# Optimization experiments

Hardware: AMD Instinct MI355X
Metric: run time of the kernel (lower is better)

Reference implementation:

```python
import jax, jax.numpy as jnp
import numpy as np

G = 4           # graphs in batch
NV_PER = 3000   # variables per graph
NC_PER = 1000   # constraints per graph
DEG = 8         # constraint neighbors per variable
D_FEAT = 64
D_HID = 128
D_OUT = 64
K_BREAK = 8     # n_breakings
EPS = 1e-5


def setup_inputs() -> dict:
    key = jax.random.key(0)
    ks = jax.random.split(key, 5)
    nv, nc = G * NV_PER, G * NC_PER
    # bipartite edges: each variable connects to DEG random constraints within its graph
    var = np.tile(np.repeat(np.arange(NV_PER), DEG), G) + np.repeat(np.arange(G) * NV_PER, NV_PER * DEG)
    con = np.asarray(jax.random.randint(ks[0], (G, NV_PER * DEG), 0, NC_PER)) + (np.arange(G) * NC_PER)[:, None]
    con = con.reshape(-1)
    edge_indices = jnp.asarray(np.stack([con, var]), dtype=jnp.int32)            # (constraint, variable)
    reversed_edge_indices = jnp.asarray(np.stack([var, con]), dtype=jnp.int32)   # (variable, constraint)
    return {
        'variable_features': jax.random.normal(ks[1], (nv, D_FEAT), jnp.float32),
        'constraint_features': jax.random.normal(ks[2], (nc, D_FEAT), jnp.float32),
        'W1': jax.random.normal(ks[3], (D_FEAT + 1, D_HID), jnp.float32) * (1.0 / np.sqrt(D_FEAT + 1)),
        'b1': jnp.zeros((D_HID,), jnp.float32),
        'W2': jax.random.normal(ks[4], (D_HID, D_OUT), jnp.float32) * (1.0 / np.sqrt(D_HID)),
        'b2': jnp.zeros((D_OUT,), jnp.float32),
        'gamma': jnp.ones((D_OUT,), jnp.float32),
        'beta': jnp.zeros((D_OUT,), jnp.float32),
        'edge_indices': edge_indices,
        'reversed_edge_indices': reversed_edge_indices,
        'n_variables_per_graph': jnp.full((G,), NV_PER, jnp.int32),
        'n_constraints_per_graph': jnp.full((G,), NC_PER, jnp.int32),
    }


def _build_adj(edge_indices, reversed_edge_indices, nv, N):
    # homogeneous symmetric bipartite adjacency + gcn_norm(add_self_loops=True)
    rows = jnp.concatenate([reversed_edge_indices[0], edge_indices[0] + nv])
    cols = jnp.concatenate([reversed_edge_indices[1] + nv, edge_indices[1]])
    deg = jax.ops.segment_sum(jnp.ones_like(rows, jnp.float32), rows, num_segments=N) + 1.0
    dinv = jax.lax.rsqrt(deg)
    edge_vals = dinv[rows] * dinv[cols]     # D^-1/2 A D^-1/2 off-diagonal
    loop_vals = dinv * dinv                  # self-loop diagonal
    return rows, cols, edge_vals, loop_vals


def _spmm(rows, cols, edge_vals, loop_vals, N, X):
    # X: (N, d) -> adj @ X
    return jax.ops.segment_sum(edge_vals[:, None] * X[cols], rows, num_segments=N) + loop_vals[:, None] * X


def _holo_forward(variable_features, constraint_features, W1, b1, W2, b2, gamma, beta,
                  rows, cols, edge_vals, loop_vals, break_idx, break_group, G_):
    nv = variable_features.shape[0]
    N = nv + constraint_features.shape[0]
    nvp = nv // G_
    X = jnp.concatenate([variable_features, constraint_features], axis=0)        # (N, d)
    B = break_idx.shape[0]
    one_hot = jax.nn.one_hot(break_idx, N, dtype=X.dtype)                        # (B, N)
    Xb = jnp.concatenate([jnp.broadcast_to(X, (B,) + X.shape), one_hot[:, :, None]], axis=-1)  # (B, N, d+1)
    spmm = lambda x: _spmm(rows, cols, edge_vals, loop_vals, N, x)
    h = jax.nn.relu(jax.lax.map(spmm, Xb @ W1 + b1))                             # (B, N, D_HID)
    out = jax.lax.map(spmm, h @ W2 + b2)                                         # (B, N, D_OUT)
    mu = out.mean(-1, keepdims=True)
    var = ((out - mu) ** 2).mean(-1, keepdims=True)
    holo = (out - mu) * jax.lax.rsqrt(var + EPS) * gamma + beta                  # LayerNorm
    set_link = holo[:, :nv, :]                                                   # r=1: tuples = variables
    global_mean = set_link.mean(0)                                               # (nv, D_OUT)
    tuple_group = jnp.repeat(jnp.arange(G_), nvp)                                # (nv,)
    group_sum = jax.ops.segment_sum(set_link, break_group, num_segments=G_)      # (G, nv, D_OUT)
    counts = jax.ops.segment_sum(jnp.ones((B,), holo.dtype), break_group, num_segments=G_)
    link = group_sum[tuple_group, jnp.arange(nv)] / jnp.maximum(counts[tuple_group], 1.0)[:, None]
    return jnp.where((counts[tuple_group] > 0)[:, None], link, global_mean)


def reference(variable_features, constraint_features, W1, b1, W2, b2, gamma, beta,
              edge_indices, reversed_edge_indices, n_variables_per_graph, n_constraints_per_graph):
    nv = variable_features.shape[0]
    nc = constraint_features.shape[0]
    N = nv + nc
    G_ = n_variables_per_graph.shape[0]
    nvp, ncp = nv // G_, nc // G_
    rows, cols, edge_vals, loop_vals = _build_adj(edge_indices, reversed_edge_indices, nv, N)
    node_degrees = jax.ops.segment_sum(edge_vals, rows, num_segments=N) + loop_vals  # adj row sums
    # per-graph top-k degree nodes (tie-expansion is measure-zero for float gcn-norm degrees)
    var_ids = jnp.arange(G_)[:, None] * nvp + jnp.arange(nvp)[None, :]
    con_ids = nv + jnp.arange(G_)[:, None] * ncp + jnp.arange(ncp)[None, :]
    sample_nodes = jnp.concatenate([var_ids, con_ids], axis=1)                   # (G, nvp+ncp)
    _, local = jax.lax.top_k(node_degrees[sample_nodes], K_BREAK)
    break_idx = jnp.take_along_axis(sample_nodes, local, axis=1).reshape(-1)     # (G*K,)
    break_group = jnp.repeat(jnp.arange(G_), K_BREAK)
    return _holo_forward(variable_features, constraint_features, W1, b1, W2, b2, gamma, beta,
                         rows, cols, edge_vals, loop_vals, break_idx, break_group, G_)
```

## Files before the change

kernel.cpp:

```cpp
#include <hip/hip_runtime.h>
#include <hip/hip_bf16.h>

#define G_      4
#define NVP     3000
#define NCP     1000
#define DEG     8
#define NV      (G_*NVP)
#define NC      (G_*NCP)
#define NN      (NV+NC)
#define NE      (NV*DEG)
#define EPG     (NVP*DEG)
#define DF      64
#define DH      128
#define DO      64
#define KB      8
#define NB      (G_*KB)
#define MAXR    96
#define MAXJ    640
#define FWD2_GEMM_BLOCKS (NV/32)

__global__ __launch_bounds__(1024) void k_setup(const int* __restrict__ conArr,
    int* __restrict__ csr_off, int* __restrict__ csr_cur,
    float* __restrict__ dinvC_g, float* __restrict__ nodeval, int* __restrict__ breakix)
{
    __shared__ int   cnt[NCP];
    __shared__ float dinvC[NCP];
    __shared__ float nvl[NVP + NCP];
    __shared__ int   wsum[16];
    __shared__ float mv[16]; __shared__ int mp[16];

    int g = blockIdx.x, tid = threadIdx.x, lane = tid & 63, w = tid >> 6;
    int ebase = g * EPG, cb = g * NCP;
    const float dv3 = 1.0f/3.0f;

    if (tid < NCP) cnt[tid] = 0;
    __syncthreads();
    for (int e = tid; e < EPG; e += 1024)
        atomicAdd(&cnt[conArr[ebase + e] - cb], 1);
    __syncthreads();
    int x = (tid < NCP) ? cnt[tid] : 0;
    int orig = x;
    for (int o = 1; o < 64; o <<= 1) { int y = __shfl_up(x, o); if (lane >= o) x += y; }
    if (lane == 63) wsum[w] = x;
    __syncthreads();
    if (tid == 0) { int run = 0; for (int t = 0; t < 16; ++t) { int z = wsum[t]; wsum[t] = run; run += z; } }
    __syncthreads();
    int excl = x - orig + wsum[w];
    if (tid < NCP) {
        csr_off[cb + tid] = ebase + excl;
        csr_cur[cb + tid] = ebase + excl;
        float dc = 1.0f / sqrtf((float)(orig + 1));
        dinvC[tid] = dc;
        dinvC_g[cb + tid] = dc;
        float nvc = (float)orig * (dc * dv3) + dc*dc;
        nvl[NVP + tid] = nvc;
        nodeval[NV + cb + tid] = nvc;
    }
    if (g == 0 && tid == 0) csr_off[NC] = NE;
    __syncthreads();
    for (int v = tid; v < NVP; v += 1024) {
        float s = 0.f;
        int e0 = ebase + v*DEG;
        #pragma unroll
        for (int k = 0; k < DEG; ++k) s += dv3 * dinvC[conArr[e0+k] - cb];
        float val = s + dv3*dv3;
        nvl[v] = val;
        nodeval[g*NVP + v] = val;
    }
    __syncthreads();
    for (int it = 0; it < KB; ++it) {
        float bv = -1e30f; int bp = 1 << 30;
        for (int p = tid; p < NVP+NCP; p += 1024) {
            float vv = nvl[p];
            if (vv > bv || (vv == bv && p < bp)) { bv = vv; bp = p; }
        }
        for (int o = 32; o > 0; o >>= 1) {
            float ov = __shfl_xor(bv, o); int op = __shfl_xor(bp, o);
            if (ov > bv || (ov == bv && op < bp)) { bv = ov; bp = op; }
        }
        if (lane == 0) { mv[w] = bv; mp[w] = bp; }
        __syncthreads();
        if (tid == 0) {
            float fv = mv[0]; int fp = mp[0];
            for (int t = 1; t < 16; ++t)
                if (mv[t] > fv || (mv[t] == fv && mp[t] < fp)) { fv = mv[t]; fp = mp[t]; }
            nvl[fp] = -1e30f;
            breakix[g*KB + it] = (fp < NVP) ? (g*NVP + fp) : (NV + g*NCP + (fp - NVP));
        }
        __syncthreads();
    }
}

__global__ __launch_bounds__(1024) void k_fill(const int* __restrict__ conArr,
                                               int* __restrict__ csr_cur,
                                               int* __restrict__ csr_v) {
    int e = blockIdx.x*1024 + threadIdx.x;
    if (e < NE) { int p = atomicAdd(&csr_cur[conArr[e]], 1); csr_v[p] = e >> 3; }
}

__global__ void k_spmmX(const float* __restrict__ vf, const float* __restrict__ cf,
                        const float* __restrict__ dinvC, const int* __restrict__ conArr,
                        const int* __restrict__ csr_off, const int* __restrict__ csr_v,
                        float* __restrict__ AX)
{
    int i = blockIdx.x*4 + (threadIdx.x >> 6);
    int lane = threadIdx.x & 63;
    const float dv3 = 1.0f/3.0f;
    float acc, di;
    if (i < NV) {
        di = dv3;
        acc = dv3 * vf[(size_t)i*DF + lane];
        int e0 = i*DEG;
        #pragma unroll
        for (int k = 0; k < DEG; ++k) {
            int c = conArr[e0+k];
            acc += dinvC[c] * cf[(size_t)c*DF + lane];
        }
    } else {
        int c = i - NV;
        di = dinvC[c];
        float base = di * cf[(size_t)c*DF + lane];
        int p0 = csr_off[c], p1 = csr_off[c+1];
        int len = p1 - p0;
        int myv = (p0 + lane < p1) ? csr_v[p0 + lane] : 0;
        int lim = len < 64 ? len : 64;
        float a0 = 0.f, a1 = 0.f, a2 = 0.f, a3 = 0.f;
        int m = 0;
        for (; m + 4 <= lim; m += 4) {
            int v0 = __shfl(myv, m+0);
            int v1 = __shfl(myv, m+1);
            int v2 = __shfl(myv, m+2);
            int v3 = __shfl(myv, m+3);
            a0 += vf[(size_t)v0*DF + lane];
            a1 += vf[(size_t)v1*DF + lane];
            a2 += vf[(size_t)v2*DF + lane];
            a3 += vf[(size_t)v3*DF + lane];
        }
        for (; m < lim; ++m) { int v = __shfl(myv, m); a0 += vf[(size_t)v*DF + lane]; }
        for (int p = p0 + 64; p < p1; ++p) a0 += vf[(size_t)csr_v[p]*DF + lane];
        acc = base + dv3 * ((a0 + a1) + (a2 + a3));
    }
    AX[(size_t)i*DF + lane] = di * acc;
}

__global__ __launch_bounds__(256) void k_gemm1(const float* __restrict__ AX, const float* __restrict__ W1,
                        const float* __restrict__ b1, const float* __restrict__ nodeval,
                        float* __restrict__ S1)
{
    __shared__ float W1T[128*68];
    __shared__ float AXs[32*68];
    int tid = threadIdx.x;
    for (int t = tid; t < 64*128; t += 256) {
        int k = t >> 7, c = t & 127;
        W1T[c*68 + k] = W1[t];
    }
    int r0 = blockIdx.x * 32;
    for (int t = tid; t < 32*16; t += 256) {
        int row = t >> 4, q = t & 15;
        *(float4*)&AXs[row*68 + q*4] = *(const float4*)&AX[(size_t)(r0+row)*DF + q*4];
    }
    __syncthreads();
    int tc = tid & 15, tr = tid >> 4;
    float acc[2][8];
    #pragma unroll
    for (int r = 0; r < 2; ++r)
        #pragma unroll
        for (int j = 0; j < 8; ++j) acc[r][j] = 0.f;
    #pragma unroll
    for (int k0 = 0; k0 < 64; k0 += 4) {
        float4 a0 = *(const float4*)&AXs[(tr*2+0)*68 + k0];
        float4 a1 = *(const float4*)&AXs[(tr*2+1)*68 + k0];
        #pragma unroll
        for (int j = 0; j < 8; ++j) {
            float4 wv = *(const float4*)&W1T[(tc + 16*j)*68 + k0];
            acc[0][j] += a0.x*wv.x + a0.y*wv.y + a0.z*wv.z + a0.w*wv.w;
            acc[1][j] += a1.x*wv.x + a1.y*wv.y + a1.z*wv.z + a1.w*wv.w;
        }
    }
    #pragma unroll
    for (int r = 0; r < 2; ++r) {
        int row = r0 + tr*2 + r;
        float nv_ = nodeval[row];
        #pragma unroll
        for (int j = 0; j < 8; ++j) {
            int col = tc + 16*j;
            S1[(size_t)row*DH + col] = acc[r][j] + nv_*b1[col];
        }
    }
}

__global__ void k_spmmH(const float* __restrict__ S1, const float* __restrict__ dinvC,
                        const int* __restrict__ conArr, float* __restrict__ AH)
{
    int v = blockIdx.x*2 + (threadIdx.x >> 7);
    int ch = threadIdx.x & 127;
    const float dv3 = 1.0f/3.0f;
    float acc = dv3 * fmaxf(S1[(size_t)v*DH + ch], 0.f);
    int e0 = v*DEG;
    #pragma unroll
    for (int k = 0; k < DEG; ++k) {
        int c = conArr[e0+k];
        acc += dinvC[c] * fmaxf(S1[(size_t)(NV + c)*DH + ch], 0.f);
    }
    AH[(size_t)v*DH + ch] = dv3 * acc;
}

__global__ __launch_bounds__(256) void k_fwd2(const float* __restrict__ S1,
    const float* __restrict__ AH,
    const float* __restrict__ dinvC, const int* __restrict__ conArr,
    const int* __restrict__ csr_off, const int* __restrict__ csr_v,
    const float* __restrict__ W1, const float* __restrict__ W2,
    const float* __restrict__ b2, const float* __restrict__ nodeval,
    const float* __restrict__ gamma, const float* __restrict__ beta,
    const int* __restrict__ breakidx,
    float* __restrict__ outvar, float* __restrict__ holo, float* __restrict__ out,
    int* __restrict__ RnG, float* __restrict__ RwG, int* __restrict__ nRG,
    float* __restrict__ dz2G)
{
    __shared__ float smem[14848];
    __shared__ int nR_s;
    int tid = threadIdx.x, lane = tid & 63, w = tid >> 6;
    const float dv3 = 1.0f/3.0f;

    if (blockIdx.x < FWD2_GEMM_BLOCKS) {
        float* W2T = smem;
        float* AHs = smem + 8448;
        float* s2  = smem + 12672;
        for (int t = tid; t < 128*64; t += 256) {
            int k = t >> 6, c = t & 63;
            W2T[c*132 + k] = W2[t];
        }
        int r0 = blockIdx.x * 32;
        for (int t = tid; t < 32*32; t += 256) {
            int row = t >> 5, q = t & 31;
            *(float4*)&AHs[row*132 + q*4] = *(const float4*)&AH[(size_t)(r0+row)*DH + q*4];
        }
        __syncthreads();
        int tc = tid & 15, tr = tid >> 4;
        float acc[2][4];
        #pragma unroll
        for (int r = 0; r < 2; ++r)
            #pragma unroll
            for (int j = 0; j < 4; ++j) acc[r][j] = 0.f;
        #pragma unroll
        for (int k0 = 0; k0 < 128; k0 += 4) {
            float4 a0 = *(const float4*)&AHs[(tr*2+0)*132 + k0];
            float4 a1 = *(const float4*)&AHs[(tr*2+1)*132 + k0];
            #pragma unroll
            for (int j = 0; j < 4; ++j) {
                float4 wv = *(const float4*)&W2T[(tc + 16*j)*132 + k0];
                acc[0][j] += a0.x*wv.x + a0.y*wv.y + a0.z*wv.z + a0.w*wv.w;
                acc[1][j] += a1.x*wv.x + a1.y*wv.y + a1.z*wv.z + a1.w*wv.w;
            }
        }
        #pragma unroll
        for (int r = 0; r < 2; ++r) {
            int row = tr*2 + r;
            float nv_ = nodeval[r0 + row];
            #pragma unroll
            for (int j = 0; j < 4; ++j) {
                int col = tc + 16*j;
                s2[row*68 + col] = acc[r][j] + nv_*b2[col];
            }
        }
        __syncthreads();
        float gm = gamma[lane], bt = beta[lane];
        for (int rr = 0; rr < 8; ++rr) {
            int row = w*8 + rr;
            int v = r0 + row;
            float xv = s2[row*68 + lane];
            float s = xv;
            for (int o = 32; o > 0; o >>= 1) s += __shfl_xor(s, o);
            float mu = s * (1.f/64.f);
            float d = xv - mu;
            float vs = d*d;
            for (int o = 32; o > 0; o >>= 1) vs += __shfl_xor(vs, o);
            float rstd = 1.0f / sqrtf(vs*(1.f/64.f) + 1e-5f);
            float h = d*rstd*gm + bt;
            outvar[(size_t)v*DO + lane] = xv;
            holo  [(size_t)v*DO + lane] = h;
            out   [(size_t)v*DO + lane] = h;
        }
    } else {
        float* W2s = smem;
        float* dh  = smem + 8192;
        float* Rw  = smem + 8704;
        int*   Rn  = (int*)(smem + 8800);
        int b = blockIdx.x - FWD2_GEMM_BLOCKS;
        int i = breakidx[b];
        for (int t = tid; t < 128*64; t += 256) W2s[t] = W2[t];
        if (tid < 64) {
            if (i >= NV) {
                int c = i - NV;
                float di = dinvC[c];
                int p0 = csr_off[c], len = csr_off[c+1] - p0;
                if (len <= 64) {
                    int v = (lane < len) ? csr_v[p0 + lane] : 0x7fffffff;
                    int firstLane = 64, mult = 0;
                    for (int m = 0; m < 64; ++m) {
                        int vm = __shfl(v, m);
                        if (vm == v) { mult++; if (m < firstLane) firstLane = m; }
                    }
                    bool head = (lane < len) && (firstLane == lane);
                    unsigned long long hmask = __ballot(head);
                    int hrk = 0;
                    for (int m = 0; m < 64; ++m) {
                        if (!((hmask >> m) & 1)) continue;
                        int vm = __shfl(v, m);
                        if (vm < v) hrk++;
                    }
                    if (head) { Rn[hrk] = v; Rw[hrk] = (float)mult * (dv3 * di); }
                    int nH = __popcll(hmask);
                    if (lane == 0) { Rn[nH] = i; Rw[nH] = di*di; nR_s = nH + 1; }
                } else if (lane == 0) {
                    int n = 0;
                    for (int p = p0; p < p0 + len; ++p) {
                        int v = csr_v[p]; int f = -1;
                        for (int q = 0; q < n; ++q) if (Rn[q] == v) { f = q; break; }
                        if (f >= 0) Rw[f] += dv3 * di;
                        else if (n < MAXR-1) { Rn[n] = v; Rw[n] = dv3 * di; ++n; }
                    }
                    Rn[n] = i; Rw[n] = di*di; nR_s = n + 1;
                }
            } else if (lane == 0) {
                float di = dv3;
                int cn[DEG];
                for (int k = 0; k < DEG; ++k) cn[k] = NV + conArr[i*DEG + k];
                for (int a = 1; a < DEG; ++a) { int key = cn[a]; int bb = a-1;
                    while (bb >= 0 && cn[bb] > key) { cn[bb+1] = cn[bb]; --bb; } cn[bb+1] = key; }
                int n = 0, k = 0;
                while (k < DEG) { int u = cn[k]; int m = 1; ++k;
                    while (k < DEG && cn[k] == u) { ++m; ++k; }
                    Rn[n] = u; Rw[n] = (float)m * dinvC[u - NV] * di; ++n; }
                Rn[n] = i; Rw[n] = di*di; nR_s = n + 1;
            }
        }
        __syncthreads();
        int nR = nR_s;
        for (int t = tid; t < nR; t += 256) { RnG[b*MAXR + t] = Rn[t]; RwG[b*MAXR + t] = Rw[t]; }
        if (tid == 0) nRG[b] = nR;
        for (int r0 = 0; r0 < nR; r0 += 4) {
            __syncthreads();
            for (int t = tid; t < 512; t += 256) {
                int ty = t >> 7, k = t & 127;
                int r = r0 + ty;
                if (r < nR) {
                    float s1 = S1[(size_t)Rn[r]*DH + k];
                    float a = s1 + Rw[r] * W1[64*128 + k];
                    dh[ty*128 + k] = fmaxf(a, 0.f) - fmaxf(s1, 0.f);
                }
            }
            __syncthreads();
            int ty2 = tid >> 6, c2 = tid & 63;
            int r2 = r0 + ty2;
            if (r2 < nR) {
                float accv = 0.f;
                #pragma unroll
                for (int kk = 0; kk < 128; ++kk) accv += dh[ty2*128 + kk] * W2s[kk*64 + c2];
                dz2G[((size_t)b*MAXR + r2)*DO + c2] = accv;
            }
        }
    }
}

__global__ __launch_bounds__(256) void k_corr_b(const int* __restrict__ RnG, const float* __restrict__ RwG,
                         const int* __restrict__ nRG, const float* __restrict__ dz2G,
                         const int* __restrict__ breakidx, const float* __restrict__ dinvC,
                         const int* __restrict__ conArr, const int* __restrict__ csr_off,
                         const int* __restrict__ csr_v,
                         const float* __restrict__ outvar, const float* __restrict__ holo,
                         const float* __restrict__ gamma, const float* __restrict__ beta,
                         float* __restrict__ out) {
    int b = blockIdx.x;
    int lane = threadIdx.x & 63, wv = threadIdx.x >> 6;
    const float dv3 = 1.0f/3.0f;
    __shared__ int Jn[MAXJ];
    __shared__ int nJ_s;
    int i = breakidx[b];
    int nR = nRG[b];
    float gm = gamma[lane], bt = beta[lane];
    if (i >= NV) {
        int nJ = nR - 1;
        const float* dzi = &dz2G[((size_t)b*MAXR + (nR-1))*DO];
        for (int j0 = wv; j0 < nJ; j0 += 4) {
            int j = RnG[b*MAXR + j0];
            float aji = RwG[b*MAXR + j0];
            float x = outvar[(size_t)j*DO + lane]
                    + aji * dzi[lane]
                    + dv3*dv3 * dz2G[((size_t)b*MAXR + j0)*DO + lane];
            float s = x; for (int o = 32; o > 0; o >>= 1) s += __shfl_xor(s, o);
            float mu = s * (1.f/64.f);
            float d = x - mu;
            float vs = d*d; for (int o = 32; o > 0; o >>= 1) vs += __shfl_xor(vs, o);
            float rstd = 1.0f / sqrtf(vs*(1.f/64.f) + 1e-5f);
            float hn = d*rstd*gm + bt;
            atomicAdd(&out[(size_t)j*DO + lane], 0.125f * (hn - holo[(size_t)j*DO + lane]));
        }
    } else {
        if (threadIdx.x == 0) {
            int n = 0; Jn[n++] = i;
            for (int r = 0; r < nR-1; ++r) {
                int c = RnG[b*MAXR + r] - NV;
                for (int p = csr_off[c]; p < csr_off[c+1]; ++p) {
                    int u = csr_v[p];
                    bool found = false;
                    for (int q = 0; q < n; ++q) if (Jn[q] == u) { found = true; break; }
                    if (!found && n < MAXJ) Jn[n++] = u;
                }
            }
            nJ_s = n;
        }
        __syncthreads();
        int nJ = nJ_s;
        for (int j0 = wv; j0 < nJ; j0 += 4) {
            int j = Jn[j0];
            float x = outvar[(size_t)j*DO + lane];
            for (int k = 0; k < DEG; ++k) {
                int cn = NV + conArr[j*DEG + k];
                for (int r = 0; r < nR-1; ++r)
                    if (RnG[b*MAXR + r] == cn) {
                        x += dv3 * dinvC[cn - NV] * dz2G[((size_t)b*MAXR + r)*DO + lane];
                        break;
                    }
            }
            if (j == i) x += dv3*dv3 * dz2G[((size_t)b*MAXR + nR-1)*DO + lane];
            float s = x; for (int o = 32; o > 0; o >>= 1) s += __shfl_xor(s, o);
            float mu = s * (1.f/64.f);
            float d = x - mu;
            float vs = d*d; for (int o = 32; o > 0; o >>= 1) vs += __shfl_xor(vs, o);
            float rstd = 1.0f / sqrtf(vs*(1.f/64.f) + 1e-5f);
            float hn = d*rstd*gm + bt;
            atomicAdd(&out[(size_t)j*DO + lane], 0.125f * (hn - holo[(size_t)j*DO + lane]));
        }
    }
}


extern "C" void kernel_launch(void* const* d_in, const int* in_sizes, int n_in,
                              void* d_out, int out_size, void* d_ws, size_t ws_size,
                              hipStream_t stream) {
    const float* vf    = (const float*)d_in[0];
    const float* cf    = (const float*)d_in[1];
    const float* W1    = (const float*)d_in[2];
    const float* b1    = (const float*)d_in[3];
    const float* W2    = (const float*)d_in[4];
    const float* b2    = (const float*)d_in[5];
    const float* gamma = (const float*)d_in[6];
    const float* beta  = (const float*)d_in[7];
    const int*   ei    = (const int*)d_in[8];
    const int*   conArr = ei;
    float* out = (float*)d_out;

    char* ws = (char*)d_ws;
    size_t off = 0;
    auto alloc = [&](size_t bytes) { char* p = ws + off; off = (off + bytes + 255) & ~(size_t)255; return p; };
    float* dinvC   = (float*)alloc(NC*4);
    int*   csr_off = (int*)  alloc((NC+1)*4);
    int*   csr_cur = (int*)  alloc(NC*4);
    int*   csr_v   = (int*)  alloc(NE*4);
    float* nodeval = (float*)alloc(NN*4);
    int*   breakix = (int*)  alloc(NB*4);
    float* AX      = (float*)alloc((size_t)NN*DF*4);
    float* S1      = (float*)alloc((size_t)NN*DH*4);
    float* AH      = (float*)alloc((size_t)NV*DH*4);
    float* outvar  = (float*)alloc((size_t)NV*DO*4);
    float* holo    = (float*)alloc((size_t)NV*DO*4);
    int*   RnG     = (int*)  alloc(NB*MAXR*4);
    float* RwG     = (float*)alloc(NB*MAXR*4);
    int*   nRG     = (int*)  alloc(NB*4);
    float* dz2G    = (float*)alloc((size_t)NB*MAXR*DO*4);

    k_setup <<<G_, 1024, 0, stream>>>(conArr, csr_off, csr_cur, dinvC, nodeval, breakix);
    k_fill  <<<(NE+1023)/1024, 1024, 0, stream>>>(conArr, csr_cur, csr_v);
    k_spmmX <<<NN/4, 256, 0, stream>>>(vf, cf, dinvC, conArr, csr_off, csr_v, AX);
    k_gemm1 <<<NN/32, 256, 0, stream>>>(AX, W1, b1, nodeval, S1);
    k_spmmH <<<NV/2, 256, 0, stream>>>(S1, dinvC, conArr, AH);
    k_fwd2  <<<FWD2_GEMM_BLOCKS + NB, 256, 0, stream>>>(S1, AH, dinvC, conArr, csr_off, csr_v,
                                       W1, W2, b2, nodeval, gamma, beta, breakix,
                                       outvar, holo, out, RnG, RwG, nRG, dz2G);
    k_corr_b<<<NB, 256, 0, stream>>>(RnG, RwG, nRG, dz2G, breakix, dinvC, conArr,
                                     csr_off, csr_v, outvar, holo, gamma, beta, out);
}
```

Before: 108.2 us.

## Fuse sparse aggregations into GEMM kernels and widen blocks to 1024 threads

Merges the feature aggregation (A·X) into the first GEMM kernel and the hidden aggregation (A·relu(H)) into the second GEMM kernel, so each 32-row tile is built in shared memory instead of going through the global AX and AH buffers. This removes two kernel launches and the global write/read round trips for those intermediates. Blocks grow to 1024 threads, with one output per thread in the GEMM stage and 8 rows per step in the correction stage. The cost is fewer resident blocks per CU, larger register and LDS pressure per block, and a dh buffer region enlarged to hold 8 rows.

After: 95.37 us, median of 2. 1.13x faster.

```diff
diff --git a/kernel.cpp b/kernel.cpp
--- a/kernel.cpp
+++ b/kernel.cpp
@@ -17,7 +17,7 @@
 #define NB      (G_*KB)
 #define MAXR    96
 #define MAXJ    640
-#define FWD2_GEMM_BLOCKS (NV/32)
+#define F2_GEMM_BLOCKS (NV/32)
 
 __global__ __launch_bounds__(1024) void k_setup(const int* __restrict__ conArr,
     int* __restrict__ csr_off, int* __restrict__ csr_cur,
@@ -98,115 +98,81 @@
     if (e < NE) { int p = atomicAdd(&csr_cur[conArr[e]], 1); csr_v[p] = e >> 3; }
 }
 
-__global__ void k_spmmX(const float* __restrict__ vf, const float* __restrict__ cf,
-                        const float* __restrict__ dinvC, const int* __restrict__ conArr,
-                        const int* __restrict__ csr_off, const int* __restrict__ csr_v,
-                        float* __restrict__ AX)
-{
-    int i = blockIdx.x*4 + (threadIdx.x >> 6);
-    int lane = threadIdx.x & 63;
-    const float dv3 = 1.0f/3.0f;
-    float acc, di;
-    if (i < NV) {
-        di = dv3;
-        acc = dv3 * vf[(size_t)i*DF + lane];
-        int e0 = i*DEG;
-        #pragma unroll
-        for (int k = 0; k < DEG; ++k) {
-            int c = conArr[e0+k];
-            acc += dinvC[c] * cf[(size_t)c*DF + lane];
-        }
-    } else {
-        int c = i - NV;
-        di = dinvC[c];
-        float base = di * cf[(size_t)c*DF + lane];
-        int p0 = csr_off[c], p1 = csr_off[c+1];
-        int len = p1 - p0;
-        int myv = (p0 + lane < p1) ? csr_v[p0 + lane] : 0;
-        int lim = len < 64 ? len : 64;
-        float a0 = 0.f, a1 = 0.f, a2 = 0.f, a3 = 0.f;
-        int m = 0;
-        for (; m + 4 <= lim; m += 4) {
-            int v0 = __shfl(myv, m+0);
-            int v1 = __shfl(myv, m+1);
-            int v2 = __shfl(myv, m+2);
-            int v3 = __shfl(myv, m+3);
-            a0 += vf[(size_t)v0*DF + lane];
-            a1 += vf[(size_t)v1*DF + lane];
-            a2 += vf[(size_t)v2*DF + lane];
-            a3 += vf[(size_t)v3*DF + lane];
-        }
-        for (; m < lim; ++m) { int v = __shfl(myv, m); a0 += vf[(size_t)v*DF + lane]; }
-        for (int p = p0 + 64; p < p1; ++p) a0 += vf[(size_t)csr_v[p]*DF + lane];
-        acc = base + dv3 * ((a0 + a1) + (a2 + a3));
-    }
-    AX[(size_t)i*DF + lane] = di * acc;
-}
-
-__global__ __launch_bounds__(256) void k_gemm1(const float* __restrict__ AX, const float* __restrict__ W1,
-                        const float* __restrict__ b1, const float* __restrict__ nodeval,
-                        float* __restrict__ S1)
+__global__ __launch_bounds__(1024) void k_f1(const float* __restrict__ vf, const float* __restrict__ cf,
+    const float* __restrict__ dinvC, const int* __restrict__ conArr,
+    const int* __restrict__ csr_off, const int* __restrict__ csr_v,
+    const float* __restrict__ W1, const float* __restrict__ b1,
+    const float* __restrict__ nodeval, float* __restrict__ S1)
 {
     __shared__ float W1T[128*68];
     __shared__ float AXs[32*68];
-    int tid = threadIdx.x;
-    for (int t = tid; t < 64*128; t += 256) {
+    int tid = threadIdx.x, lane = tid & 63, w = tid >> 6;
+    const float dv3 = 1.0f/3.0f;
+    for (int t = tid; t < 64*128; t += 1024) {
         int k = t >> 7, c = t & 127;
         W1T[c*68 + k] = W1[t];
     }
     int r0 = blockIdx.x * 32;
-    for (int t = tid; t < 32*16; t += 256) {
-        int row = t >> 4, q = t & 15;
-        *(float4*)&AXs[row*68 + q*4] = *(const float4*)&AX[(size_t)(r0+row)*DF + q*4];
+    for (int rr = w*2; rr < w*2 + 2; ++rr) {
+        int row = r0 + rr;
+        float acc, di;
+        if (row < NV) {
+            di = dv3;
+            acc = dv3 * vf[(size_t)row*DF + lane];
+            int e0 = row*DEG;
+            #pragma unroll
+            for (int k = 0; k < DEG; ++k) {
+                int c = conArr[e0+k];
+                acc += dinvC[c] * cf[(size_t)c*DF + lane];
+            }
+        } else {
+            int c = row - NV;
+            di = dinvC[c];
+            float base = di * cf[(size_t)c*DF + lane];
+            int p0 = csr_off[c], p1 = csr_off[c+1];
+            int len = p1 - p0;
+            int myv = (p0 + lane < p1) ? csr_v[p0 + lane] : 0;
+            int lim = len < 64 ? len : 64;
+            float a0 = 0.f, a1 = 0.f, a2 = 0.f, a3 = 0.f;
+            int m = 0;
+            for (; m + 4 <= lim; m += 4) {
+                int v0 = __shfl(myv, m+0);
+                int v1 = __shfl(myv, m+1);
+                int v2 = __shfl(myv, m+2);
+                int v3 = __shfl(myv, m+3);
+                a0 += vf[(size_t)v0*DF + lane];
+                a1 += vf[(size_t)v1*DF + lane];
+                a2 += vf[(size_t)v2*DF + lane];
+                a3 += vf[(size_t)v3*DF + lane];
+            }
+            for (; m < lim; ++m) { int v = __shfl(myv, m); a0 += vf[(size_t)v*DF + lane]; }
+            for (int p = p0 + 64; p < p1; ++p) a0 += vf[(size_t)csr_v[p]*DF + lane];
+            acc = base + dv3 * ((a0 + a1) + (a2 + a3));
+        }
+        AXs[rr*68 + lane] = di * acc;
     }
     __syncthreads();
     int tc = tid & 15, tr = tid >> 4;
-    float acc[2][8];
-    #pragma unroll
-    for (int r = 0; r < 2; ++r)
-        #pragma unroll
-        for (int j = 0; j < 8; ++j) acc[r][j] = 0.f;
+    int row = tr & 31, chh = tr >> 5;
+    float a4[4] = {0.f, 0.f, 0.f, 0.f};
     #pragma unroll
     for (int k0 = 0; k0 < 64; k0 += 4) {
-        float4 a0 = *(const float4*)&AXs[(tr*2+0)*68 + k0];
-        float4 a1 = *(const float4*)&AXs[(tr*2+1)*68 + k0];
+        float4 a = *(const float4*)&AXs[row*68 + k0];
         #pragma unroll
-        for (int j = 0; j < 8; ++j) {
-            float4 wv = *(const float4*)&W1T[(tc + 16*j)*68 + k0];
-            acc[0][j] += a0.x*wv.x + a0.y*wv.y + a0.z*wv.z + a0.w*wv.w;
-            acc[1][j] += a1.x*wv.x + a1.y*wv.y + a1.z*wv.z + a1.w*wv.w;
-        }
-    }
+        for (int j = 0; j < 4; ++j) {
+            float4 wv = *(const float4*)&W1T[(tc + 16*j + 64*chh)*68 + k0];
+            a4[j] += a.x*wv.x + a.y*wv.y + a.z*wv.z + a.w*wv.w;
+        }
+    }
+    float nv_ = nodeval[r0 + row];
     #pragma unroll
-    for (int r = 0; r < 2; ++r) {
-        int row = r0 + tr*2 + r;
-        float nv_ = nodeval[row];
-        #pragma unroll
-        for (int j = 0; j < 8; ++j) {
-            int col = tc + 16*j;
-            S1[(size_t)row*DH + col] = acc[r][j] + nv_*b1[col];
-        }
-    }
-}
-
-__global__ void k_spmmH(const float* __restrict__ S1, const float* __restrict__ dinvC,
-                        const int* __restrict__ conArr, float* __restrict__ AH)
-{
-    int v = blockIdx.x*2 + (threadIdx.x >> 7);
-    int ch = threadIdx.x & 127;
-    const float dv3 = 1.0f/3.0f;
-    float acc = dv3 * fmaxf(S1[(size_t)v*DH + ch], 0.f);
-    int e0 = v*DEG;
-    #pragma unroll
-    for (int k = 0; k < DEG; ++k) {
-        int c = conArr[e0+k];
-        acc += dinvC[c] * fmaxf(S1[(size_t)(NV + c)*DH + ch], 0.f);
-    }
-    AH[(size_t)v*DH + ch] = dv3 * acc;
-}
-
-__global__ __launch_bounds__(256) void k_fwd2(const float* __restrict__ S1,
-    const float* __restrict__ AH,
+    for (int j = 0; j < 4; ++j) {
+        int col = tc + 16*j + 64*chh;
+        S1[(size_t)(r0 + row)*DH + col] = a4[j] + nv_*b1[col];
+    }
+}
+
+__global__ __launch_bounds__(1024) void k_f2(const float* __restrict__ S1,
     const float* __restrict__ dinvC, const int* __restrict__ conArr,
     const int* __restrict__ csr_off, const int* __restrict__ csr_v,
     const float* __restrict__ W1, const float* __restrict__ W2,
@@ -222,53 +188,54 @@
     int tid = threadIdx.x, lane = tid & 63, w = tid >> 6;
     const float dv3 = 1.0f/3.0f;
 
-    if (blockIdx.x < FWD2_GEMM_BLOCKS) {
+    if (blockIdx.x < F2_GEMM_BLOCKS) {
         float* W2T = smem;
         float* AHs = smem + 8448;
         float* s2  = smem + 12672;
-        for (int t = tid; t < 128*64; t += 256) {
+        for (int t = tid; t < 128*64; t += 1024) {
             int k = t >> 6, c = t & 63;
             W2T[c*132 + k] = W2[t];
         }
         int r0 = blockIdx.x * 32;
-        for (int t = tid; t < 32*32; t += 256) {
-            int row = t >> 5, q = t & 31;
-            *(float4*)&AHs[row*132 + q*4] = *(const float4*)&AH[(size_t)(r0+row)*DH + q*4];
+        for (int rr = w*2; rr < w*2 + 2; ++rr) {
+            int v = r0 + rr;
+            float a0 = dv3 * fmaxf(S1[(size_t)v*DH + lane], 0.f);
+            float a1 = dv3 * fmaxf(S1[(size_t)v*DH + 64 + lane], 0.f);
+            int e0 = v*DEG;
+            #pragma unroll
+            for (int k = 0; k < DEG; ++k) {
+                int c = conArr[e0+k];
+                float dc = dinvC[c];
+                a0 += dc * fmaxf(S1[(size_t)(NV+c)*DH + lane], 0.f);
+                a1 += dc * fmaxf(S1[(size_t)(NV+c)*DH + 64 + lane], 0.f);
+            }
+            AHs[rr*132 + lane]      = dv3 * a0;
+            AHs[rr*132 + 64 + lane] = dv3 * a1;
         }
         __syncthreads();
         int tc = tid & 15, tr = tid >> 4;
-        float acc[2][4];
-        #pragma unroll
-        for (int r = 0; r < 2; ++r)
-            #pragma unroll
-            for (int j = 0; j < 4; ++j) acc[r][j] = 0.f;
+        int row = tr & 31, jh = tr >> 5;
+        float a2[2] = {0.f, 0.f};
         #pragma unroll
         for (int k0 = 0; k0 < 128; k0 += 4) {
-            float4 a0 = *(const float4*)&AHs[(tr*2+0)*132 + k0];
-            float4 a1 = *(const float4*)&AHs[(tr*2+1)*132 + k0];
+            float4 a = *(const float4*)&AHs[row*132 + k0];
             #pragma unroll
-            for (int j = 0; j < 4; ++j) {
-                float4 wv = *(const float4*)&W2T[(tc + 16*j)*132 + k0];
-                acc[0][j] += a0.x*wv.x + a0.y*wv.y + a0.z*wv.z + a0.w*wv.w;
-                acc[1][j] += a1.x*wv.x + a1.y*wv.y + a1.z*wv.z + a1.w*wv.w;
-            }
-        }
+            for (int j = 0; j < 2; ++j) {
+                float4 wv = *(const float4*)&W2T[(tc + 16*(j + 2*jh))*132 + k0];
+                a2[j] += a.x*wv.x + a.y*wv.y + a.z*wv.z + a.w*wv.w;
+            }
+        }
+        float nv_ = nodeval[r0 + row];
         #pragma unroll
-        for (int r = 0; r < 2; ++r) {
-            int row = tr*2 + r;
-            float nv_ = nodeval[r0 + row];
-            #pragma unroll
-            for (int j = 0; j < 4; ++j) {
-                int col = tc + 16*j;
-                s2[row*68 + col] = acc[r][j] + nv_*b2[col];
-            }
+        for (int j = 0; j < 2; ++j) {
+            int col = tc + 16*(j + 2*jh);
+            s2[row*68 + col] = a2[j] + nv_*b2[col];
         }
         __syncthreads();
         float gm = gamma[lane], bt = beta[lane];
-        for (int rr = 0; rr < 8; ++rr) {
-            int row = w*8 + rr;
-            int v = r0 + row;
-            float xv = s2[row*68 + lane];
+        for (int rr = w*2; rr < w*2 + 2; ++rr) {
+            int v = r0 + rr;
+            float xv = s2[rr*68 + lane];
             float s = xv;
             for (int o = 32; o > 0; o >>= 1) s += __shfl_xor(s, o);
             float mu = s * (1.f/64.f);
@@ -284,11 +251,11 @@
     } else {
         float* W2s = smem;
         float* dh  = smem + 8192;
-        float* Rw  = smem + 8704;
-        int*   Rn  = (int*)(smem + 8800);
-        int b = blockIdx.x - FWD2_GEMM_BLOCKS;
+        float* Rw  = smem + 9216;
+        int*   Rn  = (int*)(smem + 9312);
+        int b = blockIdx.x - F2_GEMM_BLOCKS;
         int i = breakidx[b];
-        for (int t = tid; t < 128*64; t += 256) W2s[t] = W2[t];
+        for (int t = tid; t < 128*64; t += 1024) W2s[t] = W2[t];
         if (tid < 64) {
             if (i >= NV) {
                 int c = i - NV;
@@ -337,13 +304,13 @@
         }
         __syncthreads();
         int nR = nR_s;
-        for (int t = tid; t < nR; t += 256) { RnG[b*MAXR + t] = Rn[t]; RwG[b*MAXR + t] = Rw[t]; }
+        for (int t = tid; t < nR; t += 1024) { RnG[b*MAXR + t] = Rn[t]; RwG[b*MAXR + t] = Rw[t]; }
         if (tid == 0) nRG[b] = nR;
-        for (int r0 = 0; r0 < nR; r0 += 4) {
+        for (int r0c = 0; r0c < nR; r0c += 8) {
             __syncthreads();
-            for (int t = tid; t < 512; t += 256) {
-                int ty = t >> 7, k = t & 127;
-                int r = r0 + ty;
+            {
+                int ty = tid >> 7, k = tid & 127;
+                int r = r0c + ty;
                 if (r < nR) {
                     float s1 = S1[(size_t)Rn[r]*DH + k];
                     float a = s1 + Rw[r] * W1[64*128 + k];
@@ -352,12 +319,14 @@
             }
             __syncthreads();
             int ty2 = tid >> 6, c2 = tid & 63;
-            int r2 = r0 + ty2;
-            if (r2 < nR) {
-                float accv = 0.f;
-                #pragma unroll
-                for (int kk = 0; kk < 128; ++kk) accv += dh[ty2*128 + kk] * W2s[kk*64 + c2];
-                dz2G[((size_t)b*MAXR + r2)*DO + c2] = accv;
+            if (ty2 < 8) {
+                int r2 = r0c + ty2;
+                if (r2 < nR) {
+                    float accv = 0.f;
+                    #pragma unroll
+                    for (int kk = 0; kk < 128; ++kk) accv += dh[ty2*128 + kk] * W2s[kk*64 + c2];
+                    dz2G[((size_t)b*MAXR + r2)*DO + c2] = accv;
+                }
             }
         }
     }
@@ -460,9 +429,7 @@
     int*   csr_v   = (int*)  alloc(NE*4);
     float* nodeval = (float*)alloc(NN*4);
     int*   breakix = (int*)  alloc(NB*4);
-    float* AX      = (float*)alloc((size_t)NN*DF*4);
     float* S1      = (float*)alloc((size_t)NN*DH*4);
-    float* AH      = (float*)alloc((size_t)NV*DH*4);
     float* outvar  = (float*)alloc((size_t)NV*DO*4);
     float* holo    = (float*)alloc((size_t)NV*DO*4);
     int*   RnG     = (int*)  alloc(NB*MAXR*4);
@@ -472,10 +439,8 @@
 
     k_setup <<<G_, 1024, 0, stream>>>(conArr, csr_off, csr_cur, dinvC, nodeval, breakix);
     k_fill  <<<(NE+1023)/1024, 1024, 0, stream>>>(conArr, csr_cur, csr_v);
-    k_spmmX <<<NN/4, 256, 0, stream>>>(vf, cf, dinvC, conArr, csr_off, csr_v, AX);
-    k_gemm1 <<<NN/32, 256, 0, stream>>>(AX, W1, b1, nodeval, S1);
-    k_spmmH <<<NV/2, 256, 0, stream>>>(S1, dinvC, conArr, AH);
-    k_fwd2  <<<FWD2_GEMM_BLOCKS + NB, 256, 0, stream>>>(S1, AH, dinvC, conArr, csr_off, csr_v,
+    k_f1    <<<NN/32, 1024, 0, stream>>>(vf, cf, dinvC, conArr, csr_off, csr_v, W1, b1, nodeval, S1);
+    k_f2    <<<F2_GEMM_BLOCKS + NB, 1024, 0, stream>>>(S1, dinvC, conArr, csr_off, csr_v,
                                        W1, W2, b2, nodeval, gamma, beta, breakix,
                                        outvar, holo, out, RnG, RwG, nRG, dz2G);
     k_corr_b<<<NB, 256, 0, stream>>>(RnG, RwG, nRG, dz2G, breakix, dinvC, conArr,
```
